# Optimization experiments

Hardware: AMD Instinct MI355X
Metric: run time of the kernel (lower is better)

The kernel has to match this reference:

```python
import jax, jax.numpy as jnp
import numpy as np
from jax import lax

DIM = 384
DIM_HEAD = 64
NUM_HEAD = DIM // DIM_HEAD
D_GROUPS = 3
NGD = DIM // D_GROUPS  # 128
KSIZE = 5
STRIDE = 2
PAD = KSIZE // 2
SCALE = DIM_HEAD ** -0.5
OFFSET_RANGE_FACTOR = 2.0
BN_EPS = 1e-6


def setup_inputs() -> dict:
    key = jax.random.key(0)
    ks = jax.random.split(key, 8)
    B, H, W = 8, 56, 56
    s = 0.02
    return {
        "x": jax.random.normal(ks[0], (B, DIM, H, W), jnp.float32),
        "q_w": jax.random.normal(ks[1], (DIM, DIM), jnp.float32) * s,
        "kv_w": jax.random.normal(ks[2], (2 * DIM, DIM), jnp.float32) * s,
        "proj_w": jax.random.normal(ks[3], (DIM, DIM), jnp.float32) * s,
        "proj_b": jnp.zeros((DIM,), jnp.float32),
        "dw_w": jax.random.normal(ks[4], (NGD, 1, KSIZE, KSIZE), jnp.float32) * s,
        "dw_b": jnp.zeros((NGD,), jnp.float32),
        "bn_w": jnp.ones((NGD,), jnp.float32),
        "bn_b": jnp.zeros((NGD,), jnp.float32),
        "bn_mean": jnp.zeros((NGD,), jnp.float32),
        "bn_var": jnp.ones((NGD,), jnp.float32),
        "pw_w": jax.random.normal(ks[5], (3, NGD), jnp.float32) * s,
    }


def grid_sample_bilinear(img, grid):
    # img: (N,C,H,W); grid: (N,Ho,Wo,2) with (x,y) in [-1,1]; align_corners=True, padding zeros
    N, C, H, W = img.shape
    gx = (grid[..., 0] + 1.0) * 0.5 * (W - 1)
    gy = (grid[..., 1] + 1.0) * 0.5 * (H - 1)
    x0 = jnp.floor(gx); y0 = jnp.floor(gy)
    x1 = x0 + 1.0; y1 = y0 + 1.0
    n_idx = jnp.arange(N)[:, None, None]

    def gather(yi, xi):
        valid = (yi >= 0) & (yi <= H - 1) & (xi >= 0) & (xi <= W - 1)
        yc = jnp.clip(yi, 0, H - 1).astype(jnp.int32)
        xc = jnp.clip(xi, 0, W - 1).astype(jnp.int32)
        v = img[n_idx, :, yc, xc]  # (N,Ho,Wo,C)
        return v * valid[..., None].astype(img.dtype)

    out = (gather(y0, x0) * ((x1 - gx) * (y1 - gy))[..., None]
           + gather(y1, x0) * ((x1 - gx) * (gy - y0))[..., None]
           + gather(y0, x1) * ((gx - x0) * (y1 - gy))[..., None]
           + gather(y1, x1) * ((gx - x0) * (gy - y0))[..., None])
    return out.transpose(0, 3, 1, 2)  # (N,C,Ho,Wo)


def _ref_points(H_off, W_off, n, dtype):
    ry = jnp.linspace(0.5, H_off - 0.5, H_off, dtype=dtype) / H_off * 2.0 - 1.0
    rx = jnp.linspace(0.5, W_off - 0.5, W_off, dtype=dtype) / W_off * 2.0 - 1.0
    ref = jnp.stack(jnp.meshgrid(ry, rx, indexing="ij"), -1)  # (Ho,Wo,2) as (y,x)
    return jnp.broadcast_to(ref[None], (n, H_off, W_off, 2))


def reference(x, q_w, kv_w, proj_w, proj_b, dw_w, dw_b, bn_w, bn_b, bn_mean, bn_var, pw_w):
    B, C, H, W = x.shape
    q = jnp.einsum("bchw,oc->bohw", x, q_w)  # 1x1 conv, no bias
    q_off = q.reshape(B * D_GROUPS, NGD, H, W)
    # depthwise conv (groups=NGD)
    off = lax.conv_general_dilated(q_off, dw_w, (STRIDE, STRIDE), [(PAD, PAD), (PAD, PAD)],
                                   feature_group_count=NGD,
                                   dimension_numbers=("NCHW", "OIHW", "NCHW"))
    off = off + dw_b[None, :, None, None]
    # BatchNorm2d (eval mode, running stats)
    off = (off - bn_mean[None, :, None, None]) * (bn_w / jnp.sqrt(bn_var + BN_EPS))[None, :, None, None] + bn_b[None, :, None, None]
    off = jax.nn.gelu(off, approximate=False)
    om = jnp.einsum("bchw,oc->bohw", off, pw_w)  # (Bg,3,Ho,Wo)
    offset, modulation = om[:, 0:2], jax.nn.sigmoid(om[:, 2:3])
    H_off, W_off = offset.shape[2], offset.shape[3]
    rng = jnp.array([1.0 / H_off, 1.0 / W_off], x.dtype).reshape(1, 2, 1, 1)
    offset = jnp.tanh(offset) * rng * OFFSET_RANGE_FACTOR
    offset = offset.transpose(0, 2, 3, 1)  # (Bg,Ho,Wo,2) as (y,x)
    pos = offset + _ref_points(H_off, W_off, B * D_GROUPS, x.dtype)
    grid = pos[..., ::-1]  # (x,y) for grid_sample
    x_s = grid_sample_bilinear(x.reshape(B * D_GROUPS, NGD, H, W), grid)
    x_s = x_s * jax.nn.sigmoid(modulation)  # note: double sigmoid as in source
    x_s = x_s.reshape(B, DIM, H_off, W_off)
    # attention
    qh = q.reshape(B, NUM_HEAD, DIM_HEAD, H * W).transpose(0, 1, 3, 2)  # (B,h,HW,d)
    kv = jnp.einsum("bchw,oc->bohw", x_s, kv_w)
    L = H_off * W_off
    kv = kv.reshape(B, 2, NUM_HEAD, DIM_HEAD, L).transpose(1, 0, 2, 4, 3)  # (2,B,h,L,d)
    k, v = kv[0], kv[1]
    attn = jax.nn.softmax(jnp.einsum("bhqd,bhkd->bhqk", qh, k) * SCALE, axis=-1)
    out = jnp.einsum("bhqk,bhkd->bhqd", attn, v)  # (B,h,HW,d)
    out = out.transpose(0, 1, 3, 2).reshape(B, DIM, H, W)
    out = jnp.einsum("bchw,oc->bohw", out, proj_w) + proj_b[None, :, None, None]
    return out
```

## Files before the change

### kernel.cpp

```cpp
#include <hip/hip_runtime.h>
#include <math.h>

#define DIMX 384
#define NHEAD 6
#define DHEAD 64
#define HW 3136
#define LKV 784
#define NGDX 128
#define NGRP 24

typedef __bf16 bf16_t;
typedef __bf16 bf16x4 __attribute__((ext_vector_type(4)));
typedef __bf16 bf16x8 __attribute__((ext_vector_type(8)));
typedef float  f32x4  __attribute__((ext_vector_type(4)));

typedef unsigned int u32_g __attribute__((address_space(1)));
typedef unsigned int u32_l __attribute__((address_space(3)));

static __device__ __forceinline__ f32x4 mfma16(bf16x8 a, bf16x8 b, f32x4 c) {
  return __builtin_amdgcn_mfma_f32_16x16x32_bf16(a, b, c, 0, 0, 0);
}
static __device__ __forceinline__ void gload16(const void* g, void* l) {
  __builtin_amdgcn_global_load_lds((const u32_g*)g, (u32_l*)l, 16, 0, 0);
}

__global__ __launch_bounds__(256) void xt_cvt(
    const float* __restrict__ x, bf16_t* __restrict__ xt)
{
  const int p0 = blockIdx.x * 64, c0 = blockIdx.y * 64, b = blockIdx.z;
  __shared__ float T[64][65];
  const int tid = threadIdx.x;
  {
    const int c = tid >> 2, pc = (tid & 3) * 16;
    const float* src = x + ((size_t)b * DIMX + c0 + c) * HW + p0 + pc;
#pragma unroll
    for (int j = 0; j < 4; ++j) {
      const float4 v = *(const float4*)(src + j * 4);
      T[c][pc + j * 4 + 0] = v.x; T[c][pc + j * 4 + 1] = v.y;
      T[c][pc + j * 4 + 2] = v.z; T[c][pc + j * 4 + 3] = v.w;
    }
  }
  __syncthreads();
  {
    const int p = tid >> 2, cc = (tid & 3) * 16;
    bf16_t* dst = xt + ((size_t)b * HW + p0 + p) * DIMX + c0 + cc;
#pragma unroll
    for (int jj = 0; jj < 2; ++jj) {
      bf16x8 o;
#pragma unroll
      for (int k = 0; k < 8; ++k) o[k] = (bf16_t)T[cc + jj * 8 + k][p];
      *(bf16x8*)(dst + jj * 8) = o;
    }
  }
}

__global__ __launch_bounds__(256) void cvt_w3(
    const float* __restrict__ qw, const float* __restrict__ kvw,
    const float* __restrict__ pw, bf16_t* __restrict__ dst)
{
  const int i = blockIdx.x * 256 + threadIdx.x;
  if (i >= 147456) return;
  const int e = i * 4;
  const float* src;
  int off;
  if (e < 147456)      { src = qw;  off = e; }
  else if (e < 442368) { src = kvw; off = e - 147456; }
  else                 { src = pw;  off = e - 442368; }
  const float4 v = *(const float4*)(src + off);
  bf16x4 o;
  o[0] = (bf16_t)v.x; o[1] = (bf16_t)v.y; o[2] = (bf16_t)v.z; o[3] = (bf16_t)v.w;
  *(bf16x4*)(dst + e) = o;
}

template<bool BIAS, bool OBF16>
__global__ __launch_bounds__(256) void gemm_qo(
    const bf16_t* __restrict__ W, const bf16_t* __restrict__ in,
    const float* __restrict__ bias, void* __restrict__ outv,
    int C, int P, int O)
{
  const int blk = blockIdx.x;
  const int y   = blk / 392;
  const int xb  = blk % 392;
  const int b   = xb / 49;
  const int o0  = y * 64;
  const int p0  = (xb % 49) * 64;
  __shared__ __align__(16) char smem[32768];
  const int tid = threadIdx.x;
  const int w = tid >> 6, lane = tid & 63, l15 = lane & 15, g = lane >> 4;
  const int lrow = lane >> 3;
  const int j    = lane & 7;

  const bf16_t* gA = W + (size_t)(o0 + w * 16 + lrow) * C + (j ^ lrow) * 8;
  const bf16_t* gB = in + ((size_t)b * P + p0 + w * 16 + lrow) * C + (j ^ lrow) * 8;

  f32x4 acc[4];
#pragma unroll
  for (int n = 0; n < 4; ++n) { acc[n][0]=0.f; acc[n][1]=0.f; acc[n][2]=0.f; acc[n][3]=0.f; }

  gload16(gA,         smem + w * 2048);
  gload16(gA + 8 * C, smem + w * 2048 + 1024);
  gload16(gB,         smem + 8192 + w * 2048);
  gload16(gB + 8 * C, smem + 8192 + w * 2048 + 1024);

  const int NK = C >> 6;
  for (int it = 0; it < NK; ++it) {
    const int buf = (it & 1) * 16384;
    __syncthreads();
    if (it + 1 < NK) {
      const int c1 = (it + 1) * 64;
      const int nb = ((it + 1) & 1) * 16384;
      gload16(gA + c1,         smem + nb + w * 2048);
      gload16(gA + c1 + 8 * C, smem + nb + w * 2048 + 1024);
      gload16(gB + c1,         smem + nb + 8192 + w * 2048);
      gload16(gB + c1 + 8 * C, smem + nb + 8192 + w * 2048 + 1024);
    }
#pragma unroll
    for (int ks = 0; ks < 2; ++ks) {
      const int cx = (ks * 64 + g * 16) ^ ((l15 & 7) << 4);
      const bf16x8 af = *(const bf16x8*)(smem + buf + (w * 16 + l15) * 128 + cx);
#pragma unroll
      for (int n = 0; n < 4; ++n) {
        const bf16x8 bfr = *(const bf16x8*)(smem + buf + 8192 + (n * 16 + l15) * 128 + cx);
        acc[n] = mfma16(af, bfr, acc[n]);
      }
    }
  }

  float badd[4];
#pragma unroll
  for (int r = 0; r < 4; ++r) badd[r] = BIAS ? bias[o0 + w * 16 + g * 4 + r] : 0.f;
#pragma unroll
  for (int n = 0; n < 4; ++n) {
    const int p = p0 + n * 16 + l15;
#pragma unroll
    for (int r = 0; r < 4; ++r) {
      const int o = o0 + w * 16 + g * 4 + r;
      const float v = acc[n][r] + badd[r];
      if (OBF16) ((bf16_t*)outv)[((size_t)b * O + o) * P + p] = (bf16_t)v;
      else       ((float*)outv)[((size_t)b * O + o) * P + p] = v;
    }
  }
}

__global__ __launch_bounds__(256) void gemm_kv(
    const bf16_t* __restrict__ W, const bf16_t* __restrict__ in,
    bf16_t* __restrict__ ktb, bf16_t* __restrict__ vtb, int C, int P, int O)
{
  const int b  = blockIdx.z;
  const int o0 = blockIdx.y * 64;
  const int p0 = blockIdx.x * 64;
  __shared__ __align__(16) bf16_t As[64][72];
  __shared__ __align__(16) bf16_t Bs[64][72];
  const int tid = threadIdx.x;
  const int w = tid >> 6, lane = tid & 63, l15 = lane & 15, g = lane >> 4;

  f32x4 acc[4];
#pragma unroll
  for (int n = 0; n < 4; ++n) { acc[n][0]=0.f; acc[n][1]=0.f; acc[n][2]=0.f; acc[n][3]=0.f; }

  for (int c0 = 0; c0 < C; c0 += 64) {
    {
      const int o = tid >> 2, cc = (tid & 3) * 16;
      const bf16_t* src = W + (size_t)(o0 + o) * C + c0 + cc;
      *(bf16x8*)&As[o][cc]     = *(const bf16x8*)src;
      *(bf16x8*)&As[o][cc + 8] = *(const bf16x8*)(src + 8);
    }
    {
      const int c = tid >> 2, pp = (tid & 3) * 16;
      const bf16_t* src = in + ((size_t)b * C + c0 + c) * P + p0 + pp;
#pragma unroll
      for (int jj = 0; jj < 2; ++jj) {
        bf16x8 v;
        if (p0 + pp + jj * 8 + 8 <= P) v = *(const bf16x8*)(src + jj * 8);
        else {
#pragma unroll
          for (int k = 0; k < 8; ++k) v[k] = (bf16_t)0.f;
        }
#pragma unroll
        for (int k = 0; k < 8; ++k) Bs[pp + jj * 8 + k][c] = v[k];
      }
    }
    __syncthreads();
#pragma unroll
    for (int ks = 0; ks < 2; ++ks) {
      const bf16x8 af = *(const bf16x8*)&As[w * 16 + l15][ks * 32 + g * 8];
#pragma unroll
      for (int n = 0; n < 4; ++n) {
        const bf16x8 bfr = *(const bf16x8*)&Bs[n * 16 + l15][ks * 32 + g * 8];
        acc[n] = mfma16(af, bfr, acc[n]);
      }
    }
    __syncthreads();
  }

  if (blockIdx.y < 6) {
    const int h = blockIdx.y;
#pragma unroll
    for (int n = 0; n < 4; ++n) {
      const int l = p0 + n * 16 + l15;
      if (l < P) {
        bf16x4 kq;
#pragma unroll
        for (int r = 0; r < 4; ++r) kq[r] = (bf16_t)acc[n][r];
        *(bf16x4*)&ktb[(((size_t)b * NHEAD + h) * LKV + l) * DHEAD + w * 16 + g * 4] = kq;
      }
    }
  } else {
#pragma unroll
    for (int n = 0; n < 4; ++n) {
      const int p = p0 + n * 16 + l15;
      if (p < P) {
#pragma unroll
        for (int r = 0; r < 4; ++r) {
          const int c = o0 - DIMX + w * 16 + g * 4 + r;
          vtb[((size_t)b * DIMX + c) * LKV + p] = (bf16_t)acc[n][r];
        }
      }
    }
  }
}

__global__ __launch_bounds__(256) void dw_bn_gelu(
    const bf16_t* __restrict__ q, const float* __restrict__ dw_w,
    const float* __restrict__ dw_b, const float* __restrict__ bn_w,
    const float* __restrict__ bn_b, const float* __restrict__ bn_mean,
    const float* __restrict__ bn_var, bf16_t* __restrict__ off)
{
  __shared__ float pl[3600];
  const int nc = blockIdx.x;
  const int c  = nc & 127;
  const bf16_t* plane = q + (size_t)nc * HW;
  const int tid = threadIdx.x;

  for (int i = tid; i < 3600; i += 256) pl[i] = 0.f;
  float w[25];
#pragma unroll
  for (int k = 0; k < 25; ++k) w[k] = dw_w[c * 25 + k];
  const float beta  = dw_b[c];
  const float scale = bn_w[c] * rsqrtf(bn_var[c] + 1e-6f);
  const float shift = bn_b[c] - bn_mean[c] * scale;
  __syncthreads();

  for (int i = tid; i < 392; i += 256) {
    const bf16x8 v = *(const bf16x8*)(plane + i * 8);
    const int y = i / 7, x0 = (i % 7) * 8;
    float* dst = &pl[(y + 2) * 60 + 2 + x0];
#pragma unroll
    for (int k = 0; k < 8; ++k) dst[k] = (float)v[k];
  }
  __syncthreads();

  for (int p = tid; p < LKV; p += 256) {
    const int oy = p / 28, ox = p % 28;
    float s = 0.f;
#pragma unroll
    for (int ky = 0; ky < 5; ++ky)
#pragma unroll
      for (int kx = 0; kx < 5; ++kx)
        s += pl[(oy * 2 + ky) * 60 + ox * 2 + kx] * w[ky * 5 + kx];
    s = (s + beta) * scale + shift;
    const float g = 0.5f * s * (1.f + erff(s * 0.70710678118654752f));
    off[(size_t)nc * LKV + p] = (bf16_t)g;
  }
}

__global__ __launch_bounds__(64) void om_grid(
    const bf16_t* __restrict__ off, const float* __restrict__ pw_w,
    float* __restrict__ gxy, float* __restrict__ modb)
{
  const int n  = blockIdx.y;
  const int lane = threadIdx.x;
  const int p  = blockIdx.x * 16 + (lane & 15);
  const int cs = lane >> 4;
  const bf16_t* base = off + (size_t)n * NGDX * LKV + p;
  float s0 = 0.f, s1 = 0.f, s2 = 0.f;
#pragma unroll 8
  for (int cc = 0; cc < 32; ++cc) {
    const int c = cs * 32 + cc;
    const float v = (float)base[(size_t)c * LKV];
    s0 += v * pw_w[c];
    s1 += v * pw_w[128 + c];
    s2 += v * pw_w[256 + c];
  }
  s0 += __shfl_xor(s0, 16); s0 += __shfl_xor(s0, 32);
  s1 += __shfl_xor(s1, 16); s1 += __shfl_xor(s1, 32);
  s2 += __shfl_xor(s2, 16); s2 += __shfl_xor(s2, 32);
  if (cs == 0) {
    const float sig1 = 1.f / (1.f + expf(-s2));
    const float mod  = 1.f / (1.f + expf(-sig1));
    const float offy = tanhf(s0) * (2.f / 28.f);
    const float offx = tanhf(s1) * (2.f / 28.f);
    const int i = p / 28, j = p % 28;
    const float refy = ((i + 0.5f) / 28.f) * 2.f - 1.f;
    const float refx = ((j + 0.5f) / 28.f) * 2.f - 1.f;
    const float gy = (offy + refy + 1.f) * 0.5f * 55.f;
    const float gx = (offx + refx + 1.f) * 0.5f * 55.f;
    gxy[((size_t)n * LKV + p) * 2 + 0] = gx;
    gxy[((size_t)n * LKV + p) * 2 + 1] = gy;
    modb[(size_t)n * LKV + p] = mod;
  }
}

__global__ __launch_bounds__(256) void sample_mod(
    const float* __restrict__ x, const float* __restrict__ gxy,
    const float* __restrict__ modb, bf16_t* __restrict__ xs)
{
  const int nc = blockIdx.x;
  const int n  = nc >> 7;
  const float* img = x + (size_t)nc * HW;
  for (int p = threadIdx.x; p < LKV; p += 256) {
    const float gx = gxy[((size_t)n * LKV + p) * 2 + 0];
    const float gy = gxy[((size_t)n * LKV + p) * 2 + 1];
    const float x0f = floorf(gx), y0f = floorf(gy);
    const float wx1 = gx - x0f, wy1 = gy - y0f;
    const float wx0 = (x0f + 1.f) - gx, wy0 = (y0f + 1.f) - gy;
    const int ix0 = (int)x0f, iy0 = (int)y0f;
    const int ix1 = ix0 + 1,  iy1 = iy0 + 1;
    const bool vx0 = (ix0 >= 0) && (ix0 < 56), vx1 = (ix1 >= 0) && (ix1 < 56);
    const bool vy0 = (iy0 >= 0) && (iy0 < 56), vy1 = (iy1 >= 0) && (iy1 < 56);
    const int cx0 = min(max(ix0, 0), 55), cx1 = min(max(ix1, 0), 55);
    const int cy0 = min(max(iy0, 0), 55), cy1 = min(max(iy1, 0), 55);
    const float f00 = (vy0 && vx0) ? img[cy0 * 56 + cx0] : 0.f;
    const float f10 = (vy1 && vx0) ? img[cy1 * 56 + cx0] : 0.f;
    const float f01 = (vy0 && vx1) ? img[cy0 * 56 + cx1] : 0.f;
    const float f11 = (vy1 && vx1) ? img[cy1 * 56 + cx1] : 0.f;
    const float v = f00 * (wx0 * wy0) + f10 * (wx0 * wy1)
                  + f01 * (wx1 * wy0) + f11 * (wx1 * wy1);
    xs[(size_t)nc * LKV + p] = (bf16_t)(v * modb[(size_t)n * LKV + p]);
  }
}

__global__ __launch_bounds__(256, 3) void attn_mfma(
    const bf16_t* __restrict__ q, const bf16_t* __restrict__ kt,
    const bf16_t* __restrict__ vt, bf16_t* __restrict__ aot)
{
  const int blk = blockIdx.x;
  const int bh  = blk % 48;
  const int t25 = blk / 48;
  const int h   = bh % NHEAD;
  const int b   = bh / NHEAD;
  const int p0  = t25 * 128;

  __shared__ __align__(16) char smem[40960];
  float (*Os)[68] = (float (*)[68])(smem);

  const int tid  = threadIdx.x;
  const int w    = tid >> 6;
  const int lane = tid & 63;
  const int l15  = lane & 15;
  const int g    = lane >> 4;
  const int lrow = lane >> 3;
  const int j    = lane & 7;

  const bf16_t* qb = q  + (size_t)(b * DIMX + h * DHEAD) * HW;
  const bf16_t* kb = kt + ((size_t)(b * NHEAD + h) * LKV) * DHEAD;
  const bf16_t* vb = vt + (size_t)(b * DIMX + h * DHEAD) * LKV;

  const bf16_t* gK = kb + (size_t)(w * 16 + lrow) * DHEAD + (j ^ lrow) * 8;
  const bf16_t* gV = vb + (size_t)(w * 16 + lrow) * LKV + (j ^ lrow) * 8;

  const float QSCL = 0.18033688011112042f;
  bf16x8 qf[2][2];
#pragma unroll
  for (int rs = 0; rs < 2; ++rs) {
    const int p = p0 + w * 32 + rs * 16 + l15;
    const bool valid = p < HW;
#pragma unroll
    for (int c2 = 0; c2 < 2; ++c2)
#pragma unroll
      for (int i = 0; i < 8; ++i) {
        const int d = c2 * 32 + g * 8 + i;
        qf[rs][c2][i] = valid ? (bf16_t)((float)qb[(size_t)d * HW + p] * QSCL) : (bf16_t)0.f;
      }
  }
  bf16x8 ones;
#pragma unroll
  for (int i = 0; i < 8; ++i) ones[i] = (bf16_t)1.0f;

  f32x4 acc[2][4];
  f32x4 lacc[2];
#pragma unroll
  for (int rs = 0; rs < 2; ++rs) {
    lacc[rs][0]=0.f; lacc[rs][1]=0.f; lacc[rs][2]=0.f; lacc[rs][3]=0.f;
#pragma unroll
    for (int n = 0; n < 4; ++n) { acc[rs][n][0]=0.f; acc[rs][n][1]=0.f; acc[rs][n][2]=0.f; acc[rs][n][3]=0.f; }
  }

  gload16(gK,                    smem + w * 2048);
  gload16(gK + (size_t)8*DHEAD,  smem + w * 2048 + 1024);
  gload16(gV,                    smem + 8192 + w * 2048);
  gload16(gV + (size_t)8*LKV,    smem + 8192 + w * 2048 + 1024);

  for (int t = 0; t < 13; ++t) {
    const int l0  = t * 64;
    const int buf = (t & 1) * 16384;
    __syncthreads();
    if (t < 12) {
      const int l1 = t * 64 + 64;
      const int nb = ((t + 1) & 1) * 16384;
      gload16(gK + (size_t)l1 * DHEAD,       smem + nb + w * 2048);
      gload16(gK + (size_t)(l1 + 8) * DHEAD, smem + nb + w * 2048 + 1024);
      gload16(gV + l1,                       smem + nb + 8192 + w * 2048);
      gload16(gV + (size_t)8 * LKV + l1,     smem + nb + 8192 + w * 2048 + 1024);
    }

    f32x4 s[2][4];
    __builtin_amdgcn_s_setprio(1);
#pragma unroll
    for (int n = 0; n < 4; ++n) {
      const int row = n * 16 + l15;
      const int cx0 = (g * 16) ^ ((l15 & 7) << 4);
      const int cx1 = (64 + g * 16) ^ ((l15 & 7) << 4);
      const bf16x8 k0 = *(const bf16x8*)(smem + buf + row * 128 + cx0);
      const bf16x8 k1 = *(const bf16x8*)(smem + buf + row * 128 + cx1);
#pragma unroll
      for (int rs = 0; rs < 2; ++rs) {
        f32x4 z; z[0]=0.f; z[1]=0.f; z[2]=0.f; z[3]=0.f;
        z = mfma16(k0, qf[rs][0], z);
        z = mfma16(k1, qf[rs][1], z);
        s[rs][n] = z;
      }
    }
    __builtin_amdgcn_s_setprio(0);
    if (l0 + 64 > LKV) {
#pragma unroll
      for (int n = 0; n < 4; ++n)
#pragma unroll
        for (int r = 0; r < 4; ++r)
          if (l0 + n * 16 + g * 4 + r >= LKV) {
#pragma unroll
            for (int rs = 0; rs < 2; ++rs) s[rs][n][r] = -1e30f;
          }
    }

    const int prow  = w * 16 + l15;
    char* pbase = smem + 32768 + prow * 128;
#pragma unroll
    for (int rs = 0; rs < 2; ++rs) {
#pragma unroll
      for (int n = 0; n < 4; ++n) {
        bf16x4 pk;
#pragma unroll
        for (int r = 0; r < 4; ++r) pk[r] = (bf16_t)exp2f(s[rs][n][r]);
        *(bf16x4*)(pbase + ((n * 32 + g * 8) ^ ((l15 & 7) << 4))) = pk;
      }
      __builtin_amdgcn_s_setprio(1);
#pragma unroll
      for (int c2 = 0; c2 < 2; ++c2) {
        bf16x8 vf[4];
#pragma unroll
        for (int n = 0; n < 4; ++n) {
          const int row = n * 16 + l15;
          const int cx = (c2 * 64 + g * 16) ^ ((l15 & 7) << 4);
          vf[n] = *(const bf16x8*)(smem + 8192 + buf + row * 128 + cx);
        }
        const bf16x8 pf = *(const bf16x8*)(pbase + ((c2 * 64 + g * 16) ^ ((l15 & 7) << 4)));
        lacc[rs] = mfma16(ones, pf, lacc[rs]);
#pragma unroll
        for (int n = 0; n < 4; ++n)
          acc[rs][n] = mfma16(vf[n], pf, acc[rs][n]);
      }
      __builtin_amdgcn_s_setprio(0);
    }
  }
  __syncthreads();

#pragma unroll
  for (int rs = 0; rs < 2; ++rs) {
    const float inv = 1.f / lacc[rs][0];
#pragma unroll
    for (int n = 0; n < 4; ++n) {
      f32x4 o4;
#pragma unroll
      for (int r = 0; r < 4; ++r) o4[r] = acc[rs][n][r] * inv;
      *(f32x4*)&Os[w * 32 + rs * 16 + l15][n * 16 + g * 4] = o4;
    }
  }
  __syncthreads();
  {
    const int pr = tid >> 1, c0 = (tid & 1) * 32;
    const int p = p0 + pr;
    if (p < HW) {
      bf16_t* dst = aot + ((size_t)b * HW + p) * DIMX + h * DHEAD + c0;
#pragma unroll
      for (int jj = 0; jj < 4; ++jj) {
        const f32x4 a = *(const f32x4*)&Os[pr][c0 + jj * 8];
        const f32x4 bq = *(const f32x4*)&Os[pr][c0 + jj * 8 + 4];
        bf16x8 o8;
        o8[0]=(bf16_t)a[0]; o8[1]=(bf16_t)a[1]; o8[2]=(bf16_t)a[2]; o8[3]=(bf16_t)a[3];
        o8[4]=(bf16_t)bq[0]; o8[5]=(bf16_t)bq[1]; o8[6]=(bf16_t)bq[2]; o8[7]=(bf16_t)bq[3];
        *(bf16x8*)(dst + jj * 8) = o8;
      }
    }
  }
}

extern "C" void kernel_launch(void* const* d_in, const int* in_sizes, int n_in,
                              void* d_out, int out_size, void* d_ws, size_t ws_size,
                              hipStream_t stream) {
  const float* x       = (const float*)d_in[0];
  const float* q_w     = (const float*)d_in[1];
  const float* kv_w    = (const float*)d_in[2];
  const float* proj_w  = (const float*)d_in[3];
  const float* proj_b  = (const float*)d_in[4];
  const float* dw_w    = (const float*)d_in[5];
  const float* dw_b    = (const float*)d_in[6];
  const float* bn_w    = (const float*)d_in[7];
  const float* bn_b    = (const float*)d_in[8];
  const float* bn_mean = (const float*)d_in[9];
  const float* bn_var  = (const float*)d_in[10];
  const float* pw_w    = (const float*)d_in[11];
  float* out = (float*)d_out;

  char* ws = (char*)d_ws;
  bf16_t* qbufb = (bf16_t*)(ws);
  bf16_t* offb  = (bf16_t*)(ws + 19267584);
  float*  gxy   = (float*)(ws + 24084480);
  float*  modb  = (float*)(ws + 24235008);
  bf16_t* ktb   = (bf16_t*)(ws + 24310272);
  bf16_t* vtb   = (bf16_t*)(ws + 29127168);
  bf16_t* xsb   = (bf16_t*)(ws + 33944064);
  bf16_t* xt    = (bf16_t*)(ws + 38760960);
  bf16_t* aot   = xt;
  bf16_t* wbf   = (bf16_t*)(ws + 58028544);
  bf16_t* q_wb  = wbf;
  bf16_t* kv_wb = wbf + 147456;
  bf16_t* pj_wb = wbf + 442368;

  const dim3 blk(256);
  xt_cvt<<<dim3(49, 6, 8), blk, 0, stream>>>(x, xt);
  cvt_w3<<<dim3(576), blk, 0, stream>>>(q_w, kv_w, proj_w, wbf);
  gemm_qo<false, true><<<dim3(2352), blk, 0, stream>>>(q_wb, xt, nullptr, qbufb, 384, 3136, 384);
  dw_bn_gelu<<<dim3(3072), blk, 0, stream>>>(qbufb, dw_w, dw_b, bn_w, bn_b, bn_mean, bn_var, offb);
  om_grid<<<dim3(49, 24), dim3(64), 0, stream>>>(offb, pw_w, gxy, modb);
  sample_mod<<<dim3(3072), blk, 0, stream>>>(x, gxy, modb, xsb);
  gemm_kv<<<dim3(13, 12, 8), blk, 0, stream>>>(kv_wb, xsb, ktb, vtb, 384, 784, 768);
  attn_mfma<<<dim3(1200), blk, 0, stream>>>(qbufb, ktb, vtb, aot);
  gemm_qo<true, false><<<dim3(2352), blk, 0, stream>>>(pj_wb, aot, proj_b, out, 384, 3136, 384);
}
```

Baseline: 156.8 us.

## Single-buffer K/V in LDS via register prefetch to raise attention occupancy

Replaces the double-buffered global_load_lds K/V pipeline with register-staged prefetch into one LDS buffer, which roughly halves shared memory. The output staging tile is stored as bf16 instead of fp32, and launch bounds rise from 3 to 5 blocks per SM. The aim is more resident waves to hide latency, at the cost of an extra barrier per tile and VGPR pressure from the prefetch registers.

```diff
diff --git a/kernel.cpp b/kernel.cpp
--- a/kernel.cpp
+++ b/kernel.cpp
@@ -330,7 +330,7 @@
   }
 }
 
-__global__ __launch_bounds__(256, 3) void attn_mfma(
+__global__ __launch_bounds__(256, 5) void attn_mfma(
     const bf16_t* __restrict__ q, const bf16_t* __restrict__ kt,
     const bf16_t* __restrict__ vt, bf16_t* __restrict__ aot)
 {
@@ -341,8 +341,8 @@
   const int b   = bh / NHEAD;
   const int p0  = t25 * 128;
 
-  __shared__ __align__(16) char smem[40960];
-  float (*Os)[68] = (float (*)[68])(smem);
+  __shared__ __align__(16) char smem[24576];
+  bf16_t (*Os)[80] = (bf16_t(*)[80])(smem);
 
   const int tid  = threadIdx.x;
   const int w    = tid >> 6;
@@ -358,6 +358,10 @@
 
   const bf16_t* gK = kb + (size_t)(w * 16 + lrow) * DHEAD + (j ^ lrow) * 8;
   const bf16_t* gV = vb + (size_t)(w * 16 + lrow) * LKV + (j ^ lrow) * 8;
+  char* kd0 = smem + w * 2048 + lane * 16;
+  char* kd1 = smem + w * 2048 + 1024 + lane * 16;
+  char* vd0 = smem + 8192 + w * 2048 + lane * 16;
+  char* vd1 = smem + 8192 + w * 2048 + 1024 + lane * 16;
 
   const float QSCL = 0.18033688011112042f;
   bf16x8 qf[2][2];
@@ -386,22 +390,25 @@
     for (int n = 0; n < 4; ++n) { acc[rs][n][0]=0.f; acc[rs][n][1]=0.f; acc[rs][n][2]=0.f; acc[rs][n][3]=0.f; }
   }
 
-  gload16(gK,                    smem + w * 2048);
-  gload16(gK + (size_t)8*DHEAD,  smem + w * 2048 + 1024);
-  gload16(gV,                    smem + 8192 + w * 2048);
-  gload16(gV + (size_t)8*LKV,    smem + 8192 + w * 2048 + 1024);
-
+  {
+    const bf16x8 k0 = *(const bf16x8*)(gK);
+    const bf16x8 k1 = *(const bf16x8*)(gK + (size_t)8 * DHEAD);
+    const bf16x8 v0 = *(const bf16x8*)(gV);
+    const bf16x8 v1 = *(const bf16x8*)(gV + (size_t)8 * LKV);
+    *(bf16x8*)kd0 = k0; *(bf16x8*)kd1 = k1;
+    *(bf16x8*)vd0 = v0; *(bf16x8*)vd1 = v1;
+  }
+  __syncthreads();
+
+  bf16x8 kr0, kr1, vr0, vr1;
   for (int t = 0; t < 13; ++t) {
-    const int l0  = t * 64;
-    const int buf = (t & 1) * 16384;
-    __syncthreads();
+    const int l0 = t * 64;
     if (t < 12) {
-      const int l1 = t * 64 + 64;
-      const int nb = ((t + 1) & 1) * 16384;
-      gload16(gK + (size_t)l1 * DHEAD,       smem + nb + w * 2048);
-      gload16(gK + (size_t)(l1 + 8) * DHEAD, smem + nb + w * 2048 + 1024);
-      gload16(gV + l1,                       smem + nb + 8192 + w * 2048);
-      gload16(gV + (size_t)8 * LKV + l1,     smem + nb + 8192 + w * 2048 + 1024);
+      const int l1 = l0 + 64;
+      kr0 = *(const bf16x8*)(gK + (size_t)l1 * DHEAD);
+      kr1 = *(const bf16x8*)(gK + (size_t)(l1 + 8) * DHEAD);
+      vr0 = *(const bf16x8*)(gV + l1);
+      vr1 = *(const bf16x8*)(gV + (size_t)8 * LKV + l1);
     }
 
     f32x4 s[2][4];
@@ -411,8 +418,8 @@
       const int row = n * 16 + l15;
       const int cx0 = (g * 16) ^ ((l15 & 7) << 4);
       const int cx1 = (64 + g * 16) ^ ((l15 & 7) << 4);
-      const bf16x8 k0 = *(const bf16x8*)(smem + buf + row * 128 + cx0);
-      const bf16x8 k1 = *(const bf16x8*)(smem + buf + row * 128 + cx1);
+      const bf16x8 k0 = *(const bf16x8*)(smem + row * 128 + cx0);
+      const bf16x8 k1 = *(const bf16x8*)(smem + row * 128 + cx1);
 #pragma unroll
       for (int rs = 0; rs < 2; ++rs) {
         f32x4 z; z[0]=0.f; z[1]=0.f; z[2]=0.f; z[3]=0.f;
@@ -434,7 +441,7 @@
     }
 
     const int prow  = w * 16 + l15;
-    char* pbase = smem + 32768 + prow * 128;
+    char* pbase = smem + 16384 + prow * 128;
 #pragma unroll
     for (int rs = 0; rs < 2; ++rs) {
 #pragma unroll
@@ -452,7 +459,7 @@
         for (int n = 0; n < 4; ++n) {
           const int row = n * 16 + l15;
           const int cx = (c2 * 64 + g * 16) ^ ((l15 & 7) << 4);
-          vf[n] = *(const bf16x8*)(smem + 8192 + buf + row * 128 + cx);
+          vf[n] = *(const bf16x8*)(smem + 8192 + row * 128 + cx);
         }
         const bf16x8 pf = *(const bf16x8*)(pbase + ((c2 * 64 + g * 16) ^ ((l15 & 7) << 4)));
         lacc[rs] = mfma16(ones, pf, lacc[rs]);
@@ -462,18 +469,24 @@
       }
       __builtin_amdgcn_s_setprio(0);
     }
-  }
-  __syncthreads();
+
+    __syncthreads();
+    if (t < 12) {
+      *(bf16x8*)kd0 = kr0; *(bf16x8*)kd1 = kr1;
+      *(bf16x8*)vd0 = vr0; *(bf16x8*)vd1 = vr1;
+      __syncthreads();
+    }
+  }
 
 #pragma unroll
   for (int rs = 0; rs < 2; ++rs) {
     const float inv = 1.f / lacc[rs][0];
 #pragma unroll
     for (int n = 0; n < 4; ++n) {
-      f32x4 o4;
-#pragma unroll
-      for (int r = 0; r < 4; ++r) o4[r] = acc[rs][n][r] * inv;
-      *(f32x4*)&Os[w * 32 + rs * 16 + l15][n * 16 + g * 4] = o4;
+      bf16x4 o4;
+#pragma unroll
+      for (int r = 0; r < 4; ++r) o4[r] = (bf16_t)(acc[rs][n][r] * inv);
+      *(bf16x4*)&Os[w * 32 + rs * 16 + l15][n * 16 + g * 4] = o4;
     }
   }
   __syncthreads();
@@ -484,12 +497,8 @@
       bf16_t* dst = aot + ((size_t)b * HW + p) * DIMX + h * DHEAD + c0;
 #pragma unroll
       for (int jj = 0; jj < 4; ++jj) {
-        const f32x4 a = *(const f32x4*)&Os[pr][c0 + jj * 8];
-        const f32x4 bq = *(const f32x4*)&Os[pr][c0 + jj * 8 + 4];
-        bf16x8 o8;
-        o8[0]=(bf16_t)a[0]; o8[1]=(bf16_t)a[1]; o8[2]=(bf16_t)a[2]; o8[3]=(bf16_t)a[3];
-        o8[4]=(bf16_t)bq[0]; o8[5]=(bf16_t)bq[1]; o8[6]=(bf16_t)bq[2]; o8[7]=(bf16_t)bq[3];
-        *(bf16x8*)(dst + jj * 8) = o8;
+        const bf16x8 v = *(const bf16x8*)&Os[pr][c0 + jj * 8];
+        *(bf16x8*)(dst + jj * 8) = v;
       }
     }
   }
```

Measured after the change: 311.9 us. 1.99x slower.
